# Optimization experiments

Hardware: AMD Instinct MI355X
Metric: run time of the kernel (lower is better)

The kernel has to match this reference:

```python
import jax, jax.numpy as jnp
import numpy as np
import math

FIRE_THRESH = 0.85
MAX_GATE = 8.0
RATE_G = 1.5
RATE_L = 2.0
EPS = 1e-12


def _gelu(x):
    c = math.sqrt(2.0 / math.pi)
    return 0.5 * x * (1.0 + jnp.tanh(c * (x + 0.044715 * x * x * x)))


def _normalize(v, axis=-1):
    n = jnp.linalg.norm(v, axis=axis, keepdims=True)
    return v / jnp.maximum(n, EPS)


def setup_inputs() -> dict:
    key = jax.random.key(0)
    k1, k2, k3 = jax.random.split(key, 3)
    B, T, D, N = 4, 4096, 1024, 512
    x = jax.random.normal(k1, (B, T, D), dtype=jnp.float32)
    buf = _normalize(jax.random.normal(k2, (N, D), dtype=jnp.float32), axis=-1)
    global_mean = _normalize(jax.random.normal(k3, (D,), dtype=jnp.float32), axis=0)[..., 0] if False else _normalize(jax.random.normal(k3, (D,), dtype=jnp.float32)[None, :], axis=-1)[0]
    return {
        "x": x,
        "log_k_local": jnp.asarray(np.log(0.5), dtype=jnp.float32),
        "log_k_global": jnp.asarray(np.log(0.5), dtype=jnp.float32),
        "buf": buf,
        "facil_l": jnp.ones((N,), dtype=jnp.float32),
        "global_mean": global_mean,
        "facil_g": jnp.asarray(1.0, dtype=jnp.float32),
        "mask": jnp.ones((N,), dtype=bool),
    }


def reference(x, log_k_local, log_k_global, buf, facil_l, global_mean, facil_g, mask):
    B, T, D = x.shape
    y = _gelu(x)

    # The torch module computes the gate entirely under no_grad / .item();
    # it is a scalar constant w.r.t. autodiff.
    y_mean = jax.lax.stop_gradient(jnp.mean(y.reshape(-1, D), axis=0))  # [D]

    m_n = y_mean / jnp.maximum(jnp.linalg.norm(y_mean), EPS)            # [D]
    buf_n = _normalize(buf, axis=-1)                                    # [N,D]
    sims_local = jnp.where(mask, buf_n @ m_n, -1.0)                     # [N]
    nearest = jnp.argmax(sims_local)
    sim_l = jnp.clip(sims_local[nearest], 0.0, 1.0)
    sim_g = jnp.clip(m_n @ global_mean, 0.0, 1.0)

    fire = sim_l > FIRE_THRESH
    facil_l_near = facil_l[nearest] * jnp.where(fire, RATE_L, 1.0)
    facil_g_new = jnp.where(fire, jnp.minimum(facil_g * RATE_G, 16.0), facil_g)

    k_l = jnp.clip(jnp.exp(log_k_local), 0.01, 4.0)
    k_g = jnp.clip(jnp.exp(log_k_global), 0.01, 4.0)

    gate = jnp.minimum(
        1.0 + k_l * (facil_l_near - 1.0) * sim_l + k_g * (facil_g_new - 1.0) * sim_g,
        MAX_GATE,
    )
    gate = jax.lax.stop_gradient(gate)
    return y * gate
```

## Files before the change

### kernel.cpp

```cpp
#include <hip/hip_runtime.h>
#include <math.h>

#define D_DIM 1024
#define N_BUF 512
#define ROWS 16384
#define TOTAL4 4194304
#define NB1 1024
#define NT1 256
#define K1_STRIDE (NB1 * NT1)
#define K1_ITERS (TOTAL4 / K1_STRIDE)

#define PART_FLOATS (NB1 * D_DIM)
#define M_OFF PART_FLOATS
#define SIMS_OFF (M_OFF + D_DIM)
#define GATE_OFF (SIMS_OFF + N_BUF)

typedef float vfloat4 __attribute__((ext_vector_type(4)));

__device__ __forceinline__ float gelu_f(float x) {
    float u = 0.7978845608028654f * (x + 0.044715f * x * x * x);
    float e = __expf(2.0f * u);
    return x * (1.0f - __builtin_amdgcn_rcpf(e + 1.0f));
}

__global__ __launch_bounds__(NT1) void k_gelu_part(
        const float* __restrict__ x, float* __restrict__ out,
        float* __restrict__ partials) {
    const int t = threadIdx.x;
    const vfloat4* __restrict__ x4 = (const vfloat4*)x;
    vfloat4* __restrict__ o4 = (vfloat4*)out;

    vfloat4 acc = (vfloat4)(0.0f);
    int idx = blockIdx.x * NT1 + t;
#pragma unroll 8
    for (int k = 0; k < K1_ITERS; ++k, idx += K1_STRIDE) {
        vfloat4 v = x4[idx];
        vfloat4 y;
        y.x = gelu_f(v.x); y.y = gelu_f(v.y); y.z = gelu_f(v.z); y.w = gelu_f(v.w);
        __builtin_nontemporal_store(y, &o4[idx]);
        acc += y;
    }
    ((vfloat4*)partials)[blockIdx.x * NT1 + t] = acc;
}

__global__ __launch_bounds__(256) void k_reduce(
        const float* __restrict__ partials, float* __restrict__ m) {
    __shared__ float red[4][64];
    const int t = threadIdx.x, sub = t >> 6, lane = t & 63;
    const int col = blockIdx.x * 64 + lane;
    const int b0 = sub * (NB1 / 4);
    float s = 0.f;
#pragma unroll 8
    for (int i = 0; i < NB1 / 4; ++i) s += partials[(b0 + i) * D_DIM + col];
    red[sub][lane] = s;
    __syncthreads();
    if (sub == 0) {
        float tot = red[0][lane] + red[1][lane] + red[2][lane] + red[3][lane];
        m[col] = tot * (1.0f / (float)ROWS);
    }
}

__device__ __forceinline__ float block_reduce_sum256(float v, float* red) {
    const int lane = threadIdx.x & 63, w = threadIdx.x >> 6;
#pragma unroll
    for (int o = 32; o > 0; o >>= 1) v += __shfl_down(v, o);
    if (lane == 0) red[w] = v;
    __syncthreads();
    float r = red[0] + red[1] + red[2] + red[3];
    __syncthreads();
    return r;
}

__global__ __launch_bounds__(256) void k_sims(
        const float* __restrict__ m, const float* __restrict__ buf,
        const unsigned char* __restrict__ mask, float* __restrict__ sims_out) {
    __shared__ float red[4];
    const int r = blockIdx.x;
    float dot = 0.f, nm2 = 0.f, nb2 = 0.f;
    for (int c = threadIdx.x; c < D_DIM; c += 256) {
        float mv = m[c];
        float b = buf[r * D_DIM + c];
        dot += b * mv;
        nm2 += mv * mv;
        nb2 += b * b;
    }
    dot = block_reduce_sum256(dot, red);
    nm2 = block_reduce_sum256(nm2, red);
    nb2 = block_reduce_sum256(nb2, red);
    if (threadIdx.x == 0) {
        float s = dot / (fmaxf(sqrtf(nm2), 1e-12f) * fmaxf(sqrtf(nb2), 1e-12f));
        sims_out[r] = mask[r] ? s : -1.0f;
    }
}

__global__ __launch_bounds__(256) void k_gate(
        const float* __restrict__ m, const float* __restrict__ sims,
        const float* __restrict__ facil_l, const float* __restrict__ gmean,
        const float* __restrict__ facil_g, const float* __restrict__ lkl,
        const float* __restrict__ lkg, float* __restrict__ gate_out) {
    __shared__ float red[4];
    __shared__ float s_best;
    __shared__ int s_bi;
    const int t = threadIdx.x, lane = t & 63, w = t >> 6;

    float nm2 = 0.f, g = 0.f;
    for (int c = t; c < D_DIM; c += 256) {
        float mv = m[c];
        nm2 += mv * mv;
        g += mv * gmean[c];
    }
    nm2 = block_reduce_sum256(nm2, red);
    g = block_reduce_sum256(g, red);

    if (w == 0) {
        float best = -2.0f; int bi = 0;
        for (int r = lane; r < N_BUF; r += 64) {
            float s = sims[r];
            if (s > best) { best = s; bi = r; }
        }
#pragma unroll
        for (int o = 32; o > 0; o >>= 1) {
            float ob = __shfl_down(best, o);
            int oi = __shfl_down(bi, o);
            if (ob > best || (ob == best && oi < bi)) { best = ob; bi = oi; }
        }
        if (lane == 0) { s_best = best; s_bi = bi; }
    }
    __syncthreads();

    if (t == 0) {
        float sim_l = fminf(fmaxf(s_best, 0.0f), 1.0f);
        float sim_g = fminf(fmaxf(g / fmaxf(sqrtf(nm2), 1e-12f), 0.0f), 1.0f);
        bool fire = sim_l > 0.85f;
        float fl = facil_l[s_bi] * (fire ? 2.0f : 1.0f);
        float fg = fire ? fminf(facil_g[0] * 1.5f, 16.0f) : facil_g[0];
        float kl = fminf(fmaxf(expf(lkl[0]), 0.01f), 4.0f);
        float kg = fminf(fmaxf(expf(lkg[0]), 0.01f), 4.0f);
        gate_out[0] = fminf(1.0f + kl * (fl - 1.0f) * sim_l + kg * (fg - 1.0f) * sim_g, 8.0f);
    }
}

__global__ __launch_bounds__(NT1) void k_scale(
        float* __restrict__ out, const float* __restrict__ gate) {
    const float gv = gate[0];
    if (gv == 1.0f) return;
    vfloat4* __restrict__ o4 = (vfloat4*)out;
    int idx = blockIdx.x * NT1 + threadIdx.x;
#pragma unroll 4
    for (int k = 0; k < K1_ITERS; ++k, idx += K1_STRIDE) {
        vfloat4 v = o4[idx];
        v *= gv;
        o4[idx] = v;
    }
}

extern "C" void kernel_launch(void* const* d_in, const int* in_sizes, int n_in,
                              void* d_out, int out_size, void* d_ws, size_t ws_size,
                              hipStream_t stream) {
    const float* x        = (const float*)d_in[0];
    const float* lkl      = (const float*)d_in[1];
    const float* lkg      = (const float*)d_in[2];
    const float* buf      = (const float*)d_in[3];
    const float* facil_l  = (const float*)d_in[4];
    const float* gmean    = (const float*)d_in[5];
    const float* facil_g  = (const float*)d_in[6];
    const unsigned char* mask = (const unsigned char*)d_in[7];
    float* out = (float*)d_out;
    float* ws  = (float*)d_ws;

    float* partials = ws;
    float* m        = ws + M_OFF;
    float* sims     = ws + SIMS_OFF;
    float* gate     = ws + GATE_OFF;

    k_gelu_part<<<dim3(NB1), dim3(NT1), 0, stream>>>(x, out, partials);
    k_reduce<<<dim3(16), dim3(256), 0, stream>>>(partials, m);
    k_sims<<<dim3(N_BUF), dim3(256), 0, stream>>>(m, buf, mask, sims);
    k_gate<<<dim3(1), dim3(256), 0, stream>>>(m, sims, facil_l, gmean,
                                              facil_g, lkl, lkg, gate);
    k_scale<<<dim3(NB1), dim3(NT1), 0, stream>>>(out, gate);
}
```

Measured before the change: 153.6 us.

## Fuse sims and gate kernels via atomic counter, widen gelu blocks, use exp2

Merges the similarity and gate kernels into one launch, where the last block (found with an atomic counter) computes the argmax and gate. The gelu pass now uses 512-thread blocks with an LDS pairwise combine of partials and an exp2-based tanh with prefolded constants. The partial reduction runs over more blocks. This is meant to cut launch overhead and make the reduction stages cheaper, at the cost of threadfence and atomic synchronisation and some changes to rounding.

```diff
diff --git a/kernel.cpp b/kernel.cpp
--- a/kernel.cpp
+++ b/kernel.cpp
@@ -6,33 +6,39 @@
 #define ROWS 16384
 #define TOTAL4 4194304
 #define NB1 1024
-#define NT1 256
+#define NT1 512
 #define K1_STRIDE (NB1 * NT1)
 #define K1_ITERS (TOTAL4 / K1_STRIDE)
+
+#define NT5 256
+#define K5_STRIDE (NB1 * NT5)
+#define K5_ITERS (TOTAL4 / K5_STRIDE)
 
 #define PART_FLOATS (NB1 * D_DIM)
 #define M_OFF PART_FLOATS
 #define SIMS_OFF (M_OFF + D_DIM)
 #define GATE_OFF (SIMS_OFF + N_BUF)
+#define CNT_OFF (GATE_OFF + 1)
 
 typedef float vfloat4 __attribute__((ext_vector_type(4)));
 
 __device__ __forceinline__ float gelu_f(float x) {
-    float u = 0.7978845608028654f * (x + 0.044715f * x * x * x);
-    float e = __expf(2.0f * u);
+    float u = x * (2.3022081f + 0.10294318f * x * x);
+    float e = __builtin_amdgcn_exp2f(u);
     return x * (1.0f - __builtin_amdgcn_rcpf(e + 1.0f));
 }
 
-__global__ __launch_bounds__(NT1) void k_gelu_part(
+__global__ __launch_bounds__(NT1, 8) void k_gelu_part(
         const float* __restrict__ x, float* __restrict__ out,
         float* __restrict__ partials) {
+    __shared__ vfloat4 lds[256];
     const int t = threadIdx.x;
     const vfloat4* __restrict__ x4 = (const vfloat4*)x;
     vfloat4* __restrict__ o4 = (vfloat4*)out;
 
     vfloat4 acc = (vfloat4)(0.0f);
     int idx = blockIdx.x * NT1 + t;
-#pragma unroll 8
+#pragma unroll 4
     for (int k = 0; k < K1_ITERS; ++k, idx += K1_STRIDE) {
         vfloat4 v = x4[idx];
         vfloat4 y;
@@ -40,24 +46,32 @@
         __builtin_nontemporal_store(y, &o4[idx]);
         acc += y;
     }
-    ((vfloat4*)partials)[blockIdx.x * NT1 + t] = acc;
+    if (t >= 256) lds[t - 256] = acc;
+    __syncthreads();
+    if (t < 256) {
+        acc += lds[t];
+        ((vfloat4*)partials)[blockIdx.x * 256 + t] = acc;
+    }
 }
 
 __global__ __launch_bounds__(256) void k_reduce(
-        const float* __restrict__ partials, float* __restrict__ m) {
-    __shared__ float red[4][64];
-    const int t = threadIdx.x, sub = t >> 6, lane = t & 63;
-    const int col = blockIdx.x * 64 + lane;
-    const int b0 = sub * (NB1 / 4);
+        const float* __restrict__ partials, float* __restrict__ m,
+        unsigned* __restrict__ cnt) {
+    __shared__ float red[8][32];
+    const int t = threadIdx.x, sub = t >> 5, lane = t & 31;
+    const int col = blockIdx.x * 32 + lane;
     float s = 0.f;
 #pragma unroll 8
-    for (int i = 0; i < NB1 / 4; ++i) s += partials[(b0 + i) * D_DIM + col];
+    for (int i = 0; i < 128; ++i) s += partials[(sub * 128 + i) * D_DIM + col];
     red[sub][lane] = s;
     __syncthreads();
-    if (sub == 0) {
-        float tot = red[0][lane] + red[1][lane] + red[2][lane] + red[3][lane];
-        m[col] = tot * (1.0f / (float)ROWS);
+    if (t < 32) {
+        float tot = 0.f;
+#pragma unroll
+        for (int j = 0; j < 8; ++j) tot += red[j][t];
+        m[blockIdx.x * 32 + t] = tot * (1.0f / (float)ROWS);
     }
+    if (blockIdx.x == 0 && t == 0) *cnt = 0u;
 }
 
 __device__ __forceinline__ float block_reduce_sum256(float v, float* red) {
@@ -71,13 +85,23 @@
     return r;
 }
 
-__global__ __launch_bounds__(256) void k_sims(
+__global__ __launch_bounds__(256) void k_simsgate(
         const float* __restrict__ m, const float* __restrict__ buf,
-        const unsigned char* __restrict__ mask, float* __restrict__ sims_out) {
+        const unsigned char* __restrict__ mask,
+        const float* __restrict__ facil_l, const float* __restrict__ gmean,
+        const float* __restrict__ facil_g, const float* __restrict__ lkl,
+        const float* __restrict__ lkg,
+        float* __restrict__ sims, float* __restrict__ gate_out,
+        unsigned* __restrict__ cnt) {
     __shared__ float red[4];
+    __shared__ bool amLast;
+    __shared__ float s_best;
+    __shared__ int s_bi;
+    const int t = threadIdx.x, lane = t & 63, w = t >> 6;
     const int r = blockIdx.x;
+
     float dot = 0.f, nm2 = 0.f, nb2 = 0.f;
-    for (int c = threadIdx.x; c < D_DIM; c += 256) {
+    for (int c = t; c < D_DIM; c += 256) {
         float mv = m[c];
         float b = buf[r * D_DIM + c];
         dot += b * mv;
@@ -87,36 +111,26 @@
     dot = block_reduce_sum256(dot, red);
     nm2 = block_reduce_sum256(nm2, red);
     nb2 = block_reduce_sum256(nb2, red);
-    if (threadIdx.x == 0) {
+    if (t == 0) {
         float s = dot / (fmaxf(sqrtf(nm2), 1e-12f) * fmaxf(sqrtf(nb2), 1e-12f));
-        sims_out[r] = mask[r] ? s : -1.0f;
+        sims[r] = mask[r] ? s : -1.0f;
     }
-}
 
-__global__ __launch_bounds__(256) void k_gate(
-        const float* __restrict__ m, const float* __restrict__ sims,
-        const float* __restrict__ facil_l, const float* __restrict__ gmean,
-        const float* __restrict__ facil_g, const float* __restrict__ lkl,
-        const float* __restrict__ lkg, float* __restrict__ gate_out) {
-    __shared__ float red[4];
-    __shared__ float s_best;
-    __shared__ int s_bi;
-    const int t = threadIdx.x, lane = t & 63, w = t >> 6;
+    __threadfence();
+    if (t == 0) amLast = (atomicAdd(cnt, 1u) == N_BUF - 1);
+    __syncthreads();
+    if (!amLast) return;
+    __threadfence();
 
-    float nm2 = 0.f, g = 0.f;
-    for (int c = t; c < D_DIM; c += 256) {
-        float mv = m[c];
-        nm2 += mv * mv;
-        g += mv * gmean[c];
-    }
-    nm2 = block_reduce_sum256(nm2, red);
+    float g = 0.f;
+    for (int c = t; c < D_DIM; c += 256) g += m[c] * gmean[c];
     g = block_reduce_sum256(g, red);
 
     if (w == 0) {
         float best = -2.0f; int bi = 0;
-        for (int r = lane; r < N_BUF; r += 64) {
-            float s = sims[r];
-            if (s > best) { best = s; bi = r; }
+        for (int i = lane; i < N_BUF; i += 64) {
+            float s = sims[i];
+            if (s > best) { best = s; bi = i; }
         }
 #pragma unroll
         for (int o = 32; o > 0; o >>= 1) {
@@ -140,14 +154,14 @@
     }
 }
 
-__global__ __launch_bounds__(NT1) void k_scale(
+__global__ __launch_bounds__(NT5) void k_scale(
         float* __restrict__ out, const float* __restrict__ gate) {
     const float gv = gate[0];
     if (gv == 1.0f) return;
     vfloat4* __restrict__ o4 = (vfloat4*)out;
-    int idx = blockIdx.x * NT1 + threadIdx.x;
+    int idx = blockIdx.x * NT5 + threadIdx.x;
 #pragma unroll 4
-    for (int k = 0; k < K1_ITERS; ++k, idx += K1_STRIDE) {
+    for (int k = 0; k < K5_ITERS; ++k, idx += K5_STRIDE) {
         vfloat4 v = o4[idx];
         v *= gv;
         o4[idx] = v;
@@ -172,11 +186,12 @@
     float* m        = ws + M_OFF;
     float* sims     = ws + SIMS_OFF;
     float* gate     = ws + GATE_OFF;
+    unsigned* cnt   = (unsigned*)(ws + CNT_OFF);
 
     k_gelu_part<<<dim3(NB1), dim3(NT1), 0, stream>>>(x, out, partials);
-    k_reduce<<<dim3(16), dim3(256), 0, stream>>>(partials, m);
-    k_sims<<<dim3(N_BUF), dim3(256), 0, stream>>>(m, buf, mask, sims);
-    k_gate<<<dim3(1), dim3(256), 0, stream>>>(m, sims, facil_l, gmean,
-                                              facil_g, lkl, lkg, gate);
-    k_scale<<<dim3(NB1), dim3(NT1), 0, stream>>>(out, gate);
+    k_reduce<<<dim3(32), dim3(256), 0, stream>>>(partials, m, cnt);
+    k_simsgate<<<dim3(N_BUF), dim3(256), 0, stream>>>(m, buf, mask, facil_l,
+                                                      gmean, facil_g, lkl, lkg,
+                                                      sims, gate, cnt);
+    k_scale<<<dim3(NB1), dim3(NT5), 0, stream>>>(out, gate);
 }
```

Result: slower. 181.6 us (+18.2%).
